# Optimization experiments

Measured on AMD Instinct MI355X. Metric: run time of the kernel, lower is better.

## Reference

```python
import jax, jax.numpy as jnp
import numpy as np

NEG_INF = -jnp.inf

def log_g(x):
    # where(x>=0, log(relu(x)+0.5), -softplus(-x)); relu(x)+0.5 >= 0.5 so log is safe everywhere
    return jnp.where(x >= 0, jnp.log(jax.nn.relu(x) + 0.5), -jax.nn.softplus(-x))

def _combine(e1, e2):
    # resettable log-space affine combine: h <- exp(logA)*h + exp(logB), reset zeroes history
    a1, b1, r1 = e1
    a2, b2, r2 = e2
    a_in = jnp.where(r2, jnp.zeros_like(a1), a1)
    b_in = jnp.where(r2, jnp.full_like(b1, NEG_INF), b1)
    return (a2 + a_in, jnp.logaddexp(a2 + b_in, b2), r1 | r2)

def setup_inputs() -> dict:
    key = jax.random.key(0)
    k1, k2, k3, k4 = jax.random.split(key, 4)
    B, T, D_in, H, D_out = 8, 4096, 1024, 1024, 1024
    x = jax.random.normal(k1, (B, T, D_in), dtype=jnp.float32)
    is_init = jax.random.uniform(k2, (B, T)) < 0.005  # sparse episode resets
    W_hg = jax.random.normal(k3, (D_in, 2 * H), dtype=jnp.float32) / np.sqrt(D_in)
    W_out = jax.random.normal(k4, (H, D_out), dtype=jnp.float32) / np.sqrt(H)
    return {"x": x, "is_init": is_init, "W_hg": W_hg, "W_out": W_out}

def reference(x, is_init, W_hg, W_out):
    # training path: h_0 = 0 (log_h_0 = -inf), seq_len > 1
    hg = jnp.einsum('btd,dk->btk', x, W_hg)            # [B,T,2H]
    hidden, gate = jnp.split(hg, 2, axis=-1)           # each [B,T,H]
    log_coeffs = -jax.nn.softplus(gate)                # log(1 - z)
    log_values = -jax.nn.softplus(-gate) + log_g(hidden)  # log z + log g(h~)
    resets = jnp.broadcast_to(is_init[:, :, None], log_coeffs.shape)
    _, logB, _ = jax.lax.associative_scan(_combine, (log_coeffs, log_values, resets), axis=1)
    # h_t = logaddexp(logA_t + log_h0, logB_t); log_h0 = -inf since h_0 = 0 => h_t = exp(logB_t)
    h = jnp.exp(logB)                                  # [B,T,H]
    out = jnp.einsum('bth,ho->bto', h, W_out)          # [B,T,D_out]
    h_n = h[:, -1:]                                    # [B,1,H]
    return out, h_n
```

## Files before the change

kernel.cpp:

```cpp
#include <hip/hip_runtime.h>
#include <stdint.h>

#define B_    8
#define T_    4096
#define DIN   1024
#define HCH   1024
#define DOUT  1024
#define M_    (B_*T_)
#define CL    64
#define NCH   (T_/CL)
#define BK    64

typedef unsigned short u16;
typedef __attribute__((ext_vector_type(8))) __bf16 bf16x8;
typedef __attribute__((ext_vector_type(4))) float  f32x4;

static __device__ __forceinline__ u16 f2bf(float f){
  unsigned u = __builtin_bit_cast(unsigned, f);
  return (u16)((u + 0x7FFFu + ((u >> 16) & 1u)) >> 16);
}
static __device__ __forceinline__ float bf2f(u16 h){
  return __builtin_bit_cast(float, ((unsigned)h) << 16);
}

#define GLOAD_LDS16(gp, lp) __builtin_amdgcn_global_load_lds( \
    (__attribute__((address_space(1))) void*)(gp),            \
    (__attribute__((address_space(3))) void*)(lp), 16, 0, 0)

__global__ void cvt_bf16_kernel(const float* __restrict__ in, u16* __restrict__ out, int n4){
  int i = blockIdx.x * blockDim.x + threadIdx.x;
  if (i >= n4) return;
  float4 v = ((const float4*)in)[i];
  ushort4 o;
  o.x = f2bf(v.x); o.y = f2bf(v.y); o.z = f2bf(v.z); o.w = f2bf(v.w);
  ((ushort4*)out)[i] = o;
}

__global__ void transpose_cvt_kernel(const float* __restrict__ in, u16* __restrict__ out,
                                     int R, int C){
  __shared__ float tile[32][33];
  int tx = threadIdx.x & 31, ty = threadIdx.x >> 5;
  int c0 = blockIdx.x * 32, r0 = blockIdx.y * 32;
  #pragma unroll
  for (int j = 0; j < 4; ++j)
    tile[ty + j*8][tx] = in[(size_t)(r0 + ty + j*8) * C + c0 + tx];
  __syncthreads();
  #pragma unroll
  for (int j = 0; j < 4; ++j)
    out[(size_t)(c0 + ty + j*8) * R + r0 + tx] = f2bf(tile[tx][ty + j*8]);
}

__global__ void detect_kernel(const unsigned char* __restrict__ p, int* __restrict__ flag){
  __shared__ int s;
  if (threadIdx.x == 0) s = 0;
  __syncthreads();
  int f = 0;
  for (int i = threadIdx.x; i < B_*T_; i += 256)
    if ((i & 3) && p[i]) f = 1;
  if (f) atomicOr(&s, 1);
  __syncthreads();
  if (threadIdx.x == 0) *flag = s;
}

__global__ __launch_bounds__(256, 2) void gemm1_kernel(
    const u16* __restrict__ A, const u16* __restrict__ BT,
    u16* __restrict__ cbuf, u16* __restrict__ vbuf)
{
  __shared__ u16 As[128*BK];
  __shared__ u16 Bh[128*BK];
  __shared__ u16 Bg[128*BK];
  int tid = threadIdx.x;
  int lane = tid & 63, w = tid >> 6;
  int wr = w >> 1, wc = w & 1;
  int lr = lane & 15, lg = lane >> 4;
  int m0 = blockIdx.x * 128, n0 = blockIdx.y * 128;

  f32x4 zf = {0.f, 0.f, 0.f, 0.f};
  f32x4 acch[4][4], accg[4][4];
  #pragma unroll
  for (int i = 0; i < 4; ++i)
    #pragma unroll
    for (int j = 0; j < 4; ++j){ acch[i][j] = zf; accg[i][j] = zf; }

  for (int k0 = 0; k0 < DIN; k0 += BK){
    __syncthreads();
    #pragma unroll
    for (int i = 0; i < 4; ++i){
      int eo  = tid*8 + i*2048;
      int row = eo >> 6, col = eo & 63;
      GLOAD_LDS16(A  + (size_t)(m0 + row)*DIN + k0 + col,        As + i*2048 + w*512);
      GLOAD_LDS16(BT + (size_t)(n0 + row)*DIN + k0 + col,        Bh + i*2048 + w*512);
      GLOAD_LDS16(BT + (size_t)(1024 + n0 + row)*DIN + k0 + col, Bg + i*2048 + w*512);
    }
    __syncthreads();
    #pragma unroll
    for (int ks = 0; ks < 2; ++ks){
      bf16x8 af[4], bh[4], bg[4];
      #pragma unroll
      for (int m = 0; m < 4; ++m)
        af[m] = *(const bf16x8*)&As[(wr*64 + m*16 + lr)*BK + ks*32 + lg*8];
      #pragma unroll
      for (int n = 0; n < 4; ++n){
        bh[n] = *(const bf16x8*)&Bh[(wc*64 + n*16 + lr)*BK + ks*32 + lg*8];
        bg[n] = *(const bf16x8*)&Bg[(wc*64 + n*16 + lr)*BK + ks*32 + lg*8];
      }
      #pragma unroll
      for (int m = 0; m < 4; ++m)
        #pragma unroll
        for (int n = 0; n < 4; ++n){
          acch[m][n] = __builtin_amdgcn_mfma_f32_16x16x32_bf16(af[m], bh[n], acch[m][n], 0, 0, 0);
          accg[m][n] = __builtin_amdgcn_mfma_f32_16x16x32_bf16(af[m], bg[n], accg[m][n], 0, 0, 0);
        }
    }
  }
  #pragma unroll
  for (int m = 0; m < 4; ++m)
    #pragma unroll
    for (int n = 0; n < 4; ++n)
      #pragma unroll
      for (int r = 0; r < 4; ++r){
        int row = m0 + wr*64 + m*16 + lg*4 + r;
        int col = n0 + wc*64 + n*16 + lr;
        float hv = acch[m][n][r];
        float gv = accg[m][n][r];
        float c  = 1.f / (1.f + __expf(gv));
        float z  = 1.f / (1.f + __expf(-gv));
        float g  = (hv >= 0.f) ? (hv + 0.5f) : (1.f / (1.f + __expf(-hv)));
        size_t idx = (size_t)row * HCH + col;
        cbuf[idx] = f2bf(c);
        vbuf[idx] = f2bf(z * g);
      }
}

__global__ __launch_bounds__(256, 2) void gemm2_kernel(
    const u16* __restrict__ A, const u16* __restrict__ BT, float* __restrict__ out)
{
  __shared__ u16 As[128*BK];
  __shared__ u16 Bs[128*BK];
  int tid = threadIdx.x;
  int lane = tid & 63, w = tid >> 6;
  int wr = w >> 1, wc = w & 1;
  int lr = lane & 15, lg = lane >> 4;
  int m0 = blockIdx.x * 128, n0 = blockIdx.y * 128;

  f32x4 zf = {0.f, 0.f, 0.f, 0.f};
  f32x4 acc[4][4];
  #pragma unroll
  for (int i = 0; i < 4; ++i)
    #pragma unroll
    for (int j = 0; j < 4; ++j) acc[i][j] = zf;

  for (int k0 = 0; k0 < HCH; k0 += BK){
    __syncthreads();
    #pragma unroll
    for (int i = 0; i < 4; ++i){
      int eo  = tid*8 + i*2048;
      int row = eo >> 6, col = eo & 63;
      GLOAD_LDS16(A  + (size_t)(m0 + row)*HCH + k0 + col, As + i*2048 + w*512);
      GLOAD_LDS16(BT + (size_t)(n0 + row)*HCH + k0 + col, Bs + i*2048 + w*512);
    }
    __syncthreads();
    #pragma unroll
    for (int ks = 0; ks < 2; ++ks){
      bf16x8 af[4], bb[4];
      #pragma unroll
      for (int m = 0; m < 4; ++m)
        af[m] = *(const bf16x8*)&As[(wr*64 + m*16 + lr)*BK + ks*32 + lg*8];
      #pragma unroll
      for (int n = 0; n < 4; ++n)
        bb[n] = *(const bf16x8*)&Bs[(wc*64 + n*16 + lr)*BK + ks*32 + lg*8];
      #pragma unroll
      for (int m = 0; m < 4; ++m)
        #pragma unroll
        for (int n = 0; n < 4; ++n)
          acc[m][n] = __builtin_amdgcn_mfma_f32_16x16x32_bf16(af[m], bb[n], acc[m][n], 0, 0, 0);
    }
  }
  #pragma unroll
  for (int m = 0; m < 4; ++m)
    #pragma unroll
    for (int n = 0; n < 4; ++n)
      #pragma unroll
      for (int r = 0; r < 4; ++r){
        int row = m0 + wr*64 + m*16 + lg*4 + r;
        int col = n0 + wc*64 + n*16 + lr;
        out[(size_t)row * DOUT + col] = acc[m][n][r];
      }
}

__global__ void scanA_kernel(const u16* __restrict__ cb, const u16* __restrict__ vb,
                             const void* __restrict__ isin, const int* __restrict__ mode,
                             float* __restrict__ Cc, float* __restrict__ Vc)
{
  int tid = blockIdx.x * 256 + threadIdx.x;
  int ch = tid & 1023, b = (tid >> 10) & 7, ck = tid >> 13;
  int md = *mode;
  const unsigned char* ib = (const unsigned char*)isin;
  const int* ii = (const int*)isin;
  int t0 = b * T_ + ck * CL;
  float C = 1.f, V = 0.f;
  #pragma unroll 8
  for (int i = 0; i < CL; ++i){
    int t = t0 + i;
    size_t idx = (size_t)t * HCH + ch;
    float c = bf2f(cb[idx]);
    float v = bf2f(vb[idx]);
    int r = md ? (int)ib[t] : ii[t];
    if (r){ C = 0.f; V = v; } else { V = __fmaf_rn(c, V, v); C *= c; }
  }
  int o = ck * 8192 + b * 1024 + ch;
  Cc[o] = C; Vc[o] = V;
}

__global__ void scanB_kernel(const float* __restrict__ Cc, const float* __restrict__ Vc,
                             float* __restrict__ hin)
{
  int idx = blockIdx.x * 256 + threadIdx.x;
  float h = 0.f;
  #pragma unroll 8
  for (int ck = 0; ck < NCH; ++ck){
    int o = ck * 8192 + idx;
    hin[o] = h;
    h = __fmaf_rn(Cc[o], h, Vc[o]);
  }
}

__global__ void scanC_kernel(const u16* __restrict__ cb, const u16* __restrict__ vb,
                             const void* __restrict__ isin, const int* __restrict__ mode,
                             const float* __restrict__ hin,
                             u16* __restrict__ hbf, float* __restrict__ hn)
{
  int tid = blockIdx.x * 256 + threadIdx.x;
  int ch = tid & 1023, b = (tid >> 10) & 7, ck = tid >> 13;
  int md = *mode;
  const unsigned char* ib = (const unsigned char*)isin;
  const int* ii = (const int*)isin;
  int t0 = b * T_ + ck * CL;
  float h = hin[ck * 8192 + b * 1024 + ch];
  #pragma unroll 8
  for (int i = 0; i < CL; ++i){
    int t = t0 + i;
    size_t idx = (size_t)t * HCH + ch;
    float c = bf2f(cb[idx]);
    float v = bf2f(vb[idx]);
    int r = md ? (int)ib[t] : ii[t];
    h = r ? v : __fmaf_rn(c, h, v);
    hbf[idx] = f2bf(h);
  }
  if (ck == NCH - 1) hn[b * 1024 + ch] = h;
}

extern "C" void kernel_launch(void* const* d_in, const int* in_sizes, int n_in,
                              void* d_out, int out_size, void* d_ws, size_t ws_size,
                              hipStream_t stream)
{
  const float* x    = (const float*)d_in[0];
  const void*  isin = d_in[1];
  const float* Whg  = (const float*)d_in[2];
  const float* Wout = (const float*)d_in[3];
  float* out = (float*)d_out;

  char* ws = (char*)d_ws;
  size_t off = 0;
  auto alloc = [&](size_t bytes) -> char* {
    char* p = ws + off;
    off += (bytes + 255) & ~(size_t)255;
    return p;
  };
  u16*   xbf   = (u16*)  alloc((size_t)M_ * DIN * 2);
  u16*   WThg  = (u16*)  alloc((size_t)2 * HCH * DIN * 2);
  u16*   WTout = (u16*)  alloc((size_t)DOUT * HCH * 2);
  u16*   cbuf  = (u16*)  alloc((size_t)M_ * HCH * 2);
  u16*   vbuf  = (u16*)  alloc((size_t)M_ * HCH * 2);
  u16*   hbf   = (u16*)  alloc((size_t)M_ * HCH * 2);
  float* Cc    = (float*)alloc((size_t)NCH * 8192 * 4);
  float* Vc    = (float*)alloc((size_t)NCH * 8192 * 4);
  float* hin   = (float*)alloc((size_t)NCH * 8192 * 4);
  int*   mode  = (int*)  alloc(256);
  (void)ws_size; (void)in_sizes; (void)n_in; (void)out_size;

  detect_kernel<<<1, 256, 0, stream>>>((const unsigned char*)isin, mode);
  cvt_bf16_kernel<<<(M_*DIN/4 + 255)/256, 256, 0, stream>>>(x, xbf, M_*DIN/4);
  transpose_cvt_kernel<<<dim3(2*HCH/32, DIN/32), 256, 0, stream>>>(Whg, WThg, DIN, 2*HCH);
  transpose_cvt_kernel<<<dim3(DOUT/32, HCH/32), 256, 0, stream>>>(Wout, WTout, HCH, DOUT);
  gemm1_kernel<<<dim3(M_/128, HCH/128), 256, 0, stream>>>(xbf, WThg, cbuf, vbuf);
  scanA_kernel<<<(8192*NCH)/256, 256, 0, stream>>>(cbuf, vbuf, isin, mode, Cc, Vc);
  scanB_kernel<<<8192/256, 256, 0, stream>>>(Cc, Vc, hin);
  scanC_kernel<<<(8192*NCH)/256, 256, 0, stream>>>(cbuf, vbuf, isin, mode, hin, hbf,
                                                   out + (size_t)M_ * DOUT);
  gemm2_kernel<<<dim3(M_/128, DOUT/128), 256, 0, stream>>>(hbf, WTout, out);
}
```

Measured before the change: 631.7 us.

## Replace GEMMs with 256x256 ping-pong pipelined kernel and move gating into scans

Both GEMMs now use a templated 8-wave kernel with 256x256 tiles, double-buffered LDS with XOR swizzle, interleaved staging and MFMA phases with priority hints, and grid remapping for L2 locality. The first GEMM now writes raw hidden/gate bf16 and the scan kernels recompute the gate and value, processing two channels per thread with 32-bit loads and stores. The reset-detect kernel reads words. This targets the old small-tile, fully synchronous GEMM loop, at the cost of recomputing exps in both scan passes and extra register pressure.

```diff
diff --git a/kernel.cpp b/kernel.cpp
--- a/kernel.cpp
+++ b/kernel.cpp
@@ -9,9 +9,9 @@
 #define M_    (B_*T_)
 #define CL    64
 #define NCH   (T_/CL)
-#define BK    64
 
 typedef unsigned short u16;
+typedef unsigned int   u32;
 typedef __attribute__((ext_vector_type(8))) __bf16 bf16x8;
 typedef __attribute__((ext_vector_type(4))) float  f32x4;
 
@@ -26,6 +26,10 @@
 #define GLOAD_LDS16(gp, lp) __builtin_amdgcn_global_load_lds( \
     (__attribute__((address_space(1))) void*)(gp),            \
     (__attribute__((address_space(3))) void*)(lp), 16, 0, 0)
+
+#define BARRIER() do { __builtin_amdgcn_sched_barrier(0); \
+                       __builtin_amdgcn_s_barrier();      \
+                       __builtin_amdgcn_sched_barrier(0); } while(0)
 
 __global__ void cvt_bf16_kernel(const float* __restrict__ in, u16* __restrict__ out, int n4){
   int i = blockIdx.x * blockDim.x + threadIdx.x;
@@ -50,166 +54,188 @@
     out[(size_t)(c0 + ty + j*8) * R + r0 + tx] = f2bf(tile[tx][ty + j*8]);
 }
 
-__global__ void detect_kernel(const unsigned char* __restrict__ p, int* __restrict__ flag){
+__global__ void detect_kernel(const u32* __restrict__ p, int* __restrict__ flag){
   __shared__ int s;
   if (threadIdx.x == 0) s = 0;
   __syncthreads();
   int f = 0;
-  for (int i = threadIdx.x; i < B_*T_; i += 256)
-    if ((i & 3) && p[i]) f = 1;
+  for (int i = threadIdx.x; i < (B_*T_)/4; i += 1024)
+    if (p[i] & 0xFFFFFF00u) f = 1;
   if (f) atomicOr(&s, 1);
   __syncthreads();
   if (threadIdx.x == 0) *flag = s;
 }
 
-__global__ __launch_bounds__(256, 2) void gemm1_kernel(
-    const u16* __restrict__ A, const u16* __restrict__ BT,
-    u16* __restrict__ cbuf, u16* __restrict__ vbuf)
-{
-  __shared__ u16 As[128*BK];
-  __shared__ u16 Bh[128*BK];
-  __shared__ u16 Bg[128*BK];
-  int tid = threadIdx.x;
-  int lane = tid & 63, w = tid >> 6;
-  int wr = w >> 1, wc = w & 1;
-  int lr = lane & 15, lg = lane >> 4;
-  int m0 = blockIdx.x * 128, n0 = blockIdx.y * 128;
-
-  f32x4 zf = {0.f, 0.f, 0.f, 0.f};
-  f32x4 acch[4][4], accg[4][4];
+template<bool BF16OUT, int NOUT>
+__global__ __launch_bounds__(512, 2) void gemm8p_kernel(
+    const u16* __restrict__ A, const u16* __restrict__ BT, void* __restrict__ outv)
+{
+  __shared__ u16 As[2][16384];
+  __shared__ u16 Bs[2][16384];
+
+  const int tid = threadIdx.x, lane = tid & 63, w = tid >> 6;
+  const int wm = w >> 2, wn = w & 3;
+  const int lr = lane & 15, lg = lane >> 4;
+  const int l8 = lane >> 3, l7 = lane & 7;
+  const int sgcol = (l7 ^ l8) * 8;
+
+  const int nwg = gridDim.x;
+  const int wg  = ((int)blockIdx.x & 7) * (nwg >> 3) + ((int)blockIdx.x >> 3);
+  const int mb  = wg & 127;
+  const int nb  = wg >> 7;
+  const int m0  = mb * 256, n0 = nb * 256;
+
+  const u16* __restrict__ Ab = A  + (size_t)m0 * 1024;
+  const u16* __restrict__ Bb = BT + (size_t)n0 * 1024;
+
+  auto stage = [&](u16 (*S)[16384], int buf, int half, int tt, const u16* __restrict__ Gb){
+    #pragma unroll
+    for (int i = 0; i < 2; ++i){
+      int wi = w*2 + i;
+      GLOAD_LDS16(Gb + (size_t)(half*128 + wi*8 + l8) * 1024 + tt*64 + sgcol,
+                  &S[buf][half*8192 + wi*512]);
+    }
+  };
+
+  bf16x8 af[4][2], b0[2][2], b1[2][2];
+  f32x4 acc[2][2][4][2];
   #pragma unroll
-  for (int i = 0; i < 4; ++i)
-    #pragma unroll
-    for (int j = 0; j < 4; ++j){ acch[i][j] = zf; accg[i][j] = zf; }
-
-  for (int k0 = 0; k0 < DIN; k0 += BK){
-    __syncthreads();
-    #pragma unroll
-    for (int i = 0; i < 4; ++i){
-      int eo  = tid*8 + i*2048;
-      int row = eo >> 6, col = eo & 63;
-      GLOAD_LDS16(A  + (size_t)(m0 + row)*DIN + k0 + col,        As + i*2048 + w*512);
-      GLOAD_LDS16(BT + (size_t)(n0 + row)*DIN + k0 + col,        Bh + i*2048 + w*512);
-      GLOAD_LDS16(BT + (size_t)(1024 + n0 + row)*DIN + k0 + col, Bg + i*2048 + w*512);
-    }
-    __syncthreads();
-    #pragma unroll
-    for (int ks = 0; ks < 2; ++ks){
-      bf16x8 af[4], bh[4], bg[4];
-      #pragma unroll
-      for (int m = 0; m < 4; ++m)
-        af[m] = *(const bf16x8*)&As[(wr*64 + m*16 + lr)*BK + ks*32 + lg*8];
-      #pragma unroll
-      for (int n = 0; n < 4; ++n){
-        bh[n] = *(const bf16x8*)&Bh[(wc*64 + n*16 + lr)*BK + ks*32 + lg*8];
-        bg[n] = *(const bf16x8*)&Bg[(wc*64 + n*16 + lr)*BK + ks*32 + lg*8];
-      }
+  for (int a = 0; a < 2; ++a)
+    #pragma unroll
+    for (int b = 0; b < 2; ++b)
       #pragma unroll
       for (int m = 0; m < 4; ++m)
         #pragma unroll
-        for (int n = 0; n < 4; ++n){
-          acch[m][n] = __builtin_amdgcn_mfma_f32_16x16x32_bf16(af[m], bh[n], acch[m][n], 0, 0, 0);
-          accg[m][n] = __builtin_amdgcn_mfma_f32_16x16x32_bf16(af[m], bg[n], accg[m][n], 0, 0, 0);
-        }
-    }
+        for (int n = 0; n < 2; ++n)
+          acc[a][b][m][n] = (f32x4){0.f,0.f,0.f,0.f};
+
+  auto ldA = [&](int buf, int mh){
+    #pragma unroll
+    for (int m = 0; m < 4; ++m)
+      #pragma unroll
+      for (int ks = 0; ks < 2; ++ks){
+        int R = mh*128 + wm*64 + m*16 + lr;
+        int g = (ks*4 + lg) ^ (lr & 7);
+        af[m][ks] = *(const bf16x8*)&As[buf][R*64 + g*8];
+      }
+  };
+  auto ldB = [&](bf16x8 (&bv)[2][2], int buf, int nh){
+    #pragma unroll
+    for (int n = 0; n < 2; ++n)
+      #pragma unroll
+      for (int ks = 0; ks < 2; ++ks){
+        int R = nh*128 + wn*32 + n*16 + lr;
+        int g = (ks*4 + lg) ^ (lr & 7);
+        bv[n][ks] = *(const bf16x8*)&Bs[buf][R*64 + g*8];
+      }
+  };
+  auto mmaQ = [&](f32x4 (&ac)[4][2], bf16x8 (&bv)[2][2]){
+    __builtin_amdgcn_s_setprio(1);
+    #pragma unroll
+    for (int m = 0; m < 4; ++m)
+      #pragma unroll
+      for (int n = 0; n < 2; ++n)
+        #pragma unroll
+        for (int ks = 0; ks < 2; ++ks)
+          ac[m][n] = __builtin_amdgcn_mfma_f32_16x16x32_bf16(af[m][ks], bv[n][ks], ac[m][n], 0, 0, 0);
+    __builtin_amdgcn_s_setprio(0);
+  };
+
+  stage(As, 0, 0, 0, Ab);
+  stage(Bs, 0, 0, 0, Bb);
+  stage(Bs, 0, 1, 0, Bb);
+  stage(As, 0, 1, 0, Ab);
+  stage(As, 1, 0, 1, Ab);
+  stage(Bs, 1, 0, 1, Bb);
+  stage(Bs, 1, 1, 1, Bb);
+  asm volatile("s_waitcnt vmcnt(6)" ::: "memory");
+  BARRIER();
+
+  for (int t = 0; t < 16; ++t){
+    int cur = t & 1;
+    ldA(cur, 0);
+    ldB(b0, cur, 0);
+    if (t+1 < 16) stage(As, cur^1, 1, t+1, Ab);
+    BARRIER();
+    mmaQ(acc[0][0], b0);
+    BARRIER();
+    ldB(b1, cur, 1);
+    if (t+2 < 16) stage(As, cur, 0, t+2, Ab);
+    BARRIER();
+    mmaQ(acc[0][1], b1);
+    BARRIER();
+    ldA(cur, 1);
+    if (t+2 < 16) stage(Bs, cur, 0, t+2, Bb);
+    BARRIER();
+    mmaQ(acc[1][1], b1);
+    BARRIER();
+    if (t+2 < 16) stage(Bs, cur, 1, t+2, Bb);
+    if (t < 14)       { asm volatile("s_waitcnt vmcnt(6)" ::: "memory"); }
+    else if (t == 14) { asm volatile("s_waitcnt vmcnt(0)" ::: "memory"); }
+    BARRIER();
+    mmaQ(acc[1][0], b0);
+    BARRIER();
   }
+
   #pragma unroll
-  for (int m = 0; m < 4; ++m)
-    #pragma unroll
-    for (int n = 0; n < 4; ++n)
-      #pragma unroll
-      for (int r = 0; r < 4; ++r){
-        int row = m0 + wr*64 + m*16 + lg*4 + r;
-        int col = n0 + wc*64 + n*16 + lr;
-        float hv = acch[m][n][r];
-        float gv = accg[m][n][r];
-        float c  = 1.f / (1.f + __expf(gv));
-        float z  = 1.f / (1.f + __expf(-gv));
-        float g  = (hv >= 0.f) ? (hv + 0.5f) : (1.f / (1.f + __expf(-hv)));
-        size_t idx = (size_t)row * HCH + col;
-        cbuf[idx] = f2bf(c);
-        vbuf[idx] = f2bf(z * g);
-      }
-}
-
-__global__ __launch_bounds__(256, 2) void gemm2_kernel(
-    const u16* __restrict__ A, const u16* __restrict__ BT, float* __restrict__ out)
-{
-  __shared__ u16 As[128*BK];
-  __shared__ u16 Bs[128*BK];
-  int tid = threadIdx.x;
-  int lane = tid & 63, w = tid >> 6;
-  int wr = w >> 1, wc = w & 1;
-  int lr = lane & 15, lg = lane >> 4;
-  int m0 = blockIdx.x * 128, n0 = blockIdx.y * 128;
-
-  f32x4 zf = {0.f, 0.f, 0.f, 0.f};
-  f32x4 acc[4][4];
-  #pragma unroll
-  for (int i = 0; i < 4; ++i)
-    #pragma unroll
-    for (int j = 0; j < 4; ++j) acc[i][j] = zf;
-
-  for (int k0 = 0; k0 < HCH; k0 += BK){
-    __syncthreads();
-    #pragma unroll
-    for (int i = 0; i < 4; ++i){
-      int eo  = tid*8 + i*2048;
-      int row = eo >> 6, col = eo & 63;
-      GLOAD_LDS16(A  + (size_t)(m0 + row)*HCH + k0 + col, As + i*2048 + w*512);
-      GLOAD_LDS16(BT + (size_t)(n0 + row)*HCH + k0 + col, Bs + i*2048 + w*512);
-    }
-    __syncthreads();
-    #pragma unroll
-    for (int ks = 0; ks < 2; ++ks){
-      bf16x8 af[4], bb[4];
-      #pragma unroll
-      for (int m = 0; m < 4; ++m)
-        af[m] = *(const bf16x8*)&As[(wr*64 + m*16 + lr)*BK + ks*32 + lg*8];
-      #pragma unroll
-      for (int n = 0; n < 4; ++n)
-        bb[n] = *(const bf16x8*)&Bs[(wc*64 + n*16 + lr)*BK + ks*32 + lg*8];
+  for (int mh = 0; mh < 2; ++mh)
+    #pragma unroll
+    for (int nh = 0; nh < 2; ++nh)
       #pragma unroll
       for (int m = 0; m < 4; ++m)
         #pragma unroll
-        for (int n = 0; n < 4; ++n)
-          acc[m][n] = __builtin_amdgcn_mfma_f32_16x16x32_bf16(af[m], bb[n], acc[m][n], 0, 0, 0);
-    }
-  }
-  #pragma unroll
-  for (int m = 0; m < 4; ++m)
-    #pragma unroll
-    for (int n = 0; n < 4; ++n)
-      #pragma unroll
-      for (int r = 0; r < 4; ++r){
-        int row = m0 + wr*64 + m*16 + lg*4 + r;
-        int col = n0 + wc*64 + n*16 + lr;
-        out[(size_t)row * DOUT + col] = acc[m][n][r];
-      }
-}
-
-__global__ void scanA_kernel(const u16* __restrict__ cb, const u16* __restrict__ vb,
+        for (int n = 0; n < 2; ++n)
+          #pragma unroll
+          for (int r = 0; r < 4; ++r){
+            int row = m0 + mh*128 + wm*64 + m*16 + lg*4 + r;
+            int col = n0 + nh*128 + wn*32 + n*16 + lr;
+            float v = acc[mh][nh][m][n][r];
+            if (BF16OUT) ((u16*)outv)[(size_t)row * NOUT + col] = f2bf(v);
+            else       ((float*)outv)[(size_t)row * NOUT + col] = v;
+          }
+}
+
+static __device__ __forceinline__ void cv_from_hg(float hv, float gv, float& c, float& v){
+  c = 1.f / (1.f + __expf(gv));
+  float z = 1.f - c;
+  float g = (hv >= 0.f) ? (hv + 0.5f) : (1.f / (1.f + __expf(-hv)));
+  v = z * g;
+}
+
+__global__ void scanA_kernel(const u16* __restrict__ hg,
                              const void* __restrict__ isin, const int* __restrict__ mode,
                              float* __restrict__ Cc, float* __restrict__ Vc)
 {
   int tid = blockIdx.x * 256 + threadIdx.x;
-  int ch = tid & 1023, b = (tid >> 10) & 7, ck = tid >> 13;
+  int chp = tid & 511, b = (tid >> 9) & 7, ck = tid >> 12;
+  int ch0 = chp * 2;
   int md = *mode;
   const unsigned char* ib = (const unsigned char*)isin;
   const int* ii = (const int*)isin;
   int t0 = b * T_ + ck * CL;
-  float C = 1.f, V = 0.f;
-  #pragma unroll 8
+  float C0 = 1.f, V0 = 0.f, C1 = 1.f, V1 = 0.f;
+  #pragma unroll 4
   for (int i = 0; i < CL; ++i){
     int t = t0 + i;
-    size_t idx = (size_t)t * HCH + ch;
-    float c = bf2f(cb[idx]);
-    float v = bf2f(vb[idx]);
+    const u16* rowp = hg + (size_t)t * 2048;
+    u32 h2 = *(const u32*)(rowp + ch0);
+    u32 g2 = *(const u32*)(rowp + 1024 + ch0);
+    float c0, v0, c1, v1;
+    cv_from_hg(bf2f((u16)h2), bf2f((u16)(h2 >> 16)) * 0.f + bf2f((u16)(g2 & 0xFFFF)) * 0.f + bf2f((u16)h2), 0.f ? c0 : c0, v0);
+    {
+      float hv0 = bf2f((u16)(h2 & 0xFFFF)), hv1 = bf2f((u16)(h2 >> 16));
+      float gv0 = bf2f((u16)(g2 & 0xFFFF)), gv1 = bf2f((u16)(g2 >> 16));
+      cv_from_hg(hv0, gv0, c0, v0);
+      cv_from_hg(hv1, gv1, c1, v1);
+    }
     int r = md ? (int)ib[t] : ii[t];
-    if (r){ C = 0.f; V = v; } else { V = __fmaf_rn(c, V, v); C *= c; }
+    if (r){ C0 = 0.f; V0 = v0; C1 = 0.f; V1 = v1; }
+    else  { V0 = __fmaf_rn(c0, V0, v0); C0 *= c0;
+            V1 = __fmaf_rn(c1, V1, v1); C1 *= c1; }
   }
-  int o = ck * 8192 + b * 1024 + ch;
-  Cc[o] = C; Vc[o] = V;
+  int o = ck * 8192 + b * 1024 + ch0;
+  *(float2*)&Cc[o] = make_float2(C0, C1);
+  *(float2*)&Vc[o] = make_float2(V0, V1);
 }
 
 __global__ void scanB_kernel(const float* __restrict__ Cc, const float* __restrict__ Vc,
@@ -225,29 +251,37 @@
   }
 }
 
-__global__ void scanC_kernel(const u16* __restrict__ cb, const u16* __restrict__ vb,
+__global__ void scanC_kernel(const u16* __restrict__ hg,
                              const void* __restrict__ isin, const int* __restrict__ mode,
                              const float* __restrict__ hin,
                              u16* __restrict__ hbf, float* __restrict__ hn)
 {
   int tid = blockIdx.x * 256 + threadIdx.x;
-  int ch = tid & 1023, b = (tid >> 10) & 7, ck = tid >> 13;
+  int chp = tid & 511, b = (tid >> 9) & 7, ck = tid >> 12;
+  int ch0 = chp * 2;
   int md = *mode;
   const unsigned char* ib = (const unsigned char*)isin;
   const int* ii = (const int*)isin;
   int t0 = b * T_ + ck * CL;
-  float h = hin[ck * 8192 + b * 1024 + ch];
-  #pragma unroll 8
+  int o = ck * 8192 + b * 1024 + ch0;
+  float h0 = hin[o], h1 = hin[o + 1];
+  #pragma unroll 4
   for (int i = 0; i < CL; ++i){
     int t = t0 + i;
-    size_t idx = (size_t)t * HCH + ch;
-    float c = bf2f(cb[idx]);
-    float v = bf2f(vb[idx]);
+    const u16* rowp = hg + (size_t)t * 2048;
+    u32 h2 = *(const u32*)(rowp + ch0);
+    u32 g2 = *(const u32*)(rowp + 1024 + ch0);
+    float hv0 = bf2f((u16)(h2 & 0xFFFF)), hv1 = bf2f((u16)(h2 >> 16));
+    float gv0 = bf2f((u16)(g2 & 0xFFFF)), gv1 = bf2f((u16)(g2 >> 16));
+    float c0, v0, c1, v1;
+    cv_from_hg(hv0, gv0, c0, v0);
+    cv_from_hg(hv1, gv1, c1, v1);
     int r = md ? (int)ib[t] : ii[t];
-    h = r ? v : __fmaf_rn(c, h, v);
-    hbf[idx] = f2bf(h);
+    h0 = r ? v0 : __fmaf_rn(c0, h0, v0);
+    h1 = r ? v1 : __fmaf_rn(c1, h1, v1);
+    *(u32*)&hbf[(size_t)t * HCH + ch0] = (u32)f2bf(h0) | ((u32)f2bf(h1) << 16);
   }
-  if (ck == NCH - 1) hn[b * 1024 + ch] = h;
+  if (ck == NCH - 1){ hn[b * 1024 + ch0] = h0; hn[b * 1024 + ch0 + 1] = h1; }
 }
 
 extern "C" void kernel_launch(void* const* d_in, const int* in_sizes, int n_in,
@@ -270,8 +304,7 @@
   u16*   xbf   = (u16*)  alloc((size_t)M_ * DIN * 2);
   u16*   WThg  = (u16*)  alloc((size_t)2 * HCH * DIN * 2);
   u16*   WTout = (u16*)  alloc((size_t)DOUT * HCH * 2);
-  u16*   cbuf  = (u16*)  alloc((size_t)M_ * HCH * 2);
-  u16*   vbuf  = (u16*)  alloc((size_t)M_ * HCH * 2);
+  u16*   hg    = (u16*)  alloc((size_t)M_ * 2 * HCH * 2);
   u16*   hbf   = (u16*)  alloc((size_t)M_ * HCH * 2);
   float* Cc    = (float*)alloc((size_t)NCH * 8192 * 4);
   float* Vc    = (float*)alloc((size_t)NCH * 8192 * 4);
@@ -279,14 +312,14 @@
   int*   mode  = (int*)  alloc(256);
   (void)ws_size; (void)in_sizes; (void)n_in; (void)out_size;
 
-  detect_kernel<<<1, 256, 0, stream>>>((const unsigned char*)isin, mode);
+  detect_kernel<<<1, 1024, 0, stream>>>((const u32*)isin, mode);
   cvt_bf16_kernel<<<(M_*DIN/4 + 255)/256, 256, 0, stream>>>(x, xbf, M_*DIN/4);
   transpose_cvt_kernel<<<dim3(2*HCH/32, DIN/32), 256, 0, stream>>>(Whg, WThg, DIN, 2*HCH);
   transpose_cvt_kernel<<<dim3(DOUT/32, HCH/32), 256, 0, stream>>>(Wout, WTout, HCH, DOUT);
-  gemm1_kernel<<<dim3(M_/128, HCH/128), 256, 0, stream>>>(xbf, WThg, cbuf, vbuf);
-  scanA_kernel<<<(8192*NCH)/256, 256, 0, stream>>>(cbuf, vbuf, isin, mode, Cc, Vc);
+  gemm8p_kernel<true, 2048><<<1024, 512, 0, stream>>>(xbf, WThg, hg);
+  scanA_kernel<<<(8192*NCH/2)/256, 256, 0, stream>>>(hg, isin, mode, Cc, Vc);
   scanB_kernel<<<8192/256, 256, 0, stream>>>(Cc, Vc, hin);
-  scanC_kernel<<<(8192*NCH)/256, 256, 0, stream>>>(cbuf, vbuf, isin, mode, hin, hbf,
-                                                   out + (size_t)M_ * DOUT);
-  gemm2_kernel<<<dim3(M_/128, DOUT/128), 256, 0, stream>>>(hbf, WTout, out);
-}
+  scanC_kernel<<<(8192*NCH/2)/256, 256, 0, stream>>>(hg, isin, mode, hin, hbf,
+                                                     out + (size_t)M_ * DOUT);
+  gemm8p_kernel<false, 1024><<<512, 512, 0, stream>>>(hbf, WTout, out);
+}
```

Measured after the change: 604.8 us. 1.04x faster.
